# Optimization experiments

Measured on AMD Instinct MI355X. Metric: run time of the kernel, lower is better.

## Reference

```python
import jax, jax.numpy as jnp
import numpy as np

T, E, K, H, I = 512, 16, 4, 2880, 2880
G_H, G_I = H // 32, I // 32  # MXFP4 groups of 32 values (16 bytes/block)
ALPHA, LIMIT, EPS = 1.702, 7.0, 1e-5

FP4_VALUES = jnp.array([0.0, 0.5, 1.0, 1.5, 2.0, 3.0, 4.0, 6.0,
                        -0.0, -0.5, -1.0, -1.5, -2.0, -3.0, -4.0, -6.0], jnp.float32)


def dequant_mxfp4(blocks, scales):
    # blocks: uint8 [..., G, 16]; scales: uint8 [..., G] (biased exponent)
    pre = blocks.shape[:-2]
    G, B = blocks.shape[-2], blocks.shape[-1]
    lo = FP4_VALUES[(blocks & 0xF).astype(jnp.int32)]   # [..., G, B]
    hi = FP4_VALUES[(blocks >> 4).astype(jnp.int32)]    # [..., G, B]
    vals = jnp.stack([lo, hi], axis=-1).reshape(*pre, G, B * 2)  # interleave lo/hi per byte
    vals = jnp.ldexp(vals, (scales.astype(jnp.int32) - 127)[..., None])
    return vals.reshape(*pre, G * B * 2)


def swiglu(h):
    g = jnp.minimum(h[..., 0::2], LIMIT)
    l = jnp.clip(h[..., 1::2], -LIMIT, LIMIT)
    return g * jax.nn.sigmoid(ALPHA * g) * (l + 1.0)


def setup_inputs() -> dict:
    key = jax.random.key(0)
    ks = jax.random.split(key, 10)
    x = jax.random.normal(ks[0], (T, H), jnp.float32)
    norm_scale = jnp.ones((H,), jnp.float32)
    gate_w = jax.random.normal(ks[1], (E, H), jnp.float32) * 0.02
    gate_b = jnp.zeros((E,), jnp.float32)
    mlp1_blocks = jax.random.randint(ks[2], (E, 2 * I, G_H, 16), 0, 256, dtype=jnp.uint8)
    mlp1_scales = jax.random.randint(ks[3], (E, 2 * I, G_H), 118, 128, dtype=jnp.uint8)
    mlp1_bias = jax.random.normal(ks[4], (E, 2 * I), jnp.float32) * 0.02
    mlp2_blocks = jax.random.randint(ks[5], (E, H, G_I, 16), 0, 256, dtype=jnp.uint8)
    mlp2_scales = jax.random.randint(ks[6], (E, H, G_I), 118, 128, dtype=jnp.uint8)
    mlp2_bias = jax.random.normal(ks[7], (E, H), jnp.float32) * 0.02
    return {"x": x, "norm_scale": norm_scale, "gate_w": gate_w, "gate_b": gate_b,
            "mlp1_blocks": mlp1_blocks, "mlp1_scales": mlp1_scales, "mlp1_bias": mlp1_bias,
            "mlp2_blocks": mlp2_blocks, "mlp2_scales": mlp2_scales, "mlp2_bias": mlp2_bias}


def reference(x, norm_scale, gate_w, gate_b, mlp1_blocks, mlp1_scales, mlp1_bias,
              mlp2_blocks, mlp2_scales, mlp2_bias):
    # RMSNorm
    t = x * jax.lax.rsqrt(jnp.mean(x * x, axis=-1, keepdims=True) + EPS) * norm_scale
    # router: top-k + softmax over selected logits
    g = t @ gate_w.T + gate_b                      # [T, E]
    vals, idx = jax.lax.top_k(g, K)                # sorted, distinct indices
    w = jax.nn.softmax(vals, axis=-1)              # [T, K]
    n_tok = t.shape[0]
    route = jnp.zeros((n_tok, gate_w.shape[0]), t.dtype)
    route = route.at[jnp.arange(n_tok)[:, None], idx].set(w)  # [T, E] sparse weights
    # expert MLPs (dense dispatch; unrouted experts get zero weight)
    W1 = dequant_mxfp4(mlp1_blocks, mlp1_scales)   # [E, 2I, H]
    h = jnp.einsum('th,ech->tec', t, W1) + mlp1_bias[None]   # [T, E, 2I]
    h = swiglu(h)                                            # [T, E, I]
    W2 = dequant_mxfp4(mlp2_blocks, mlp2_scales)   # [E, H, I]
    o = jnp.einsum('tec,ehc->teh', h, W2) + mlp2_bias[None]  # [T, E, H]
    return x + jnp.einsum('teh,te->th', o, route)
```

## Files before the change

kernel.cpp:

```cpp
#include <hip/hip_runtime.h>
#include <hip/hip_bf16.h>

typedef __attribute__((ext_vector_type(8))) short short8;
typedef __attribute__((ext_vector_type(4))) float f32x4;
typedef __attribute__((ext_vector_type(4))) int i32x4;
typedef __attribute__((ext_vector_type(2))) int i32x2;
typedef __attribute__((ext_vector_type(4))) unsigned u32x4;

#define NTOK 512
#define NEXP 16
#define TOPK 4
#define HD   2880
#define ID   2880
#define N1   5760
#define NGRP 90
#define NKT  45
#define ROWB 5760

__device__ __forceinline__ unsigned perm(unsigned hi, unsigned lo, unsigned sel) {
  return __builtin_amdgcn_perm(hi, lo, sel);
}

__device__ __forceinline__ u32x4 dq_word4(unsigned p, unsigned hbl, unsigned hbh,
                                          unsigned lbl, unsigned lbh) {
  unsigned ph = p >> 4;
  unsigned il = p  & 0x07070707u, sl = p  & 0x08080808u;
  unsigned ih = ph & 0x07070707u, sh = ph & 0x08080808u;
  unsigned hbL = perm(hbh, hbl, il) | (sl << 4);
  unsigned lbL = perm(lbh, lbl, il);
  unsigned hbH = perm(hbh, hbl, ih) | (sh << 4);
  unsigned lbH = perm(lbh, lbl, ih);
  unsigned mL01 = perm(hbL, lbL, 0x05010400u);
  unsigned mL23 = perm(hbL, lbL, 0x07030602u);
  unsigned mH01 = perm(hbH, lbH, 0x05010400u);
  unsigned mH23 = perm(hbH, lbH, 0x07030602u);
  u32x4 w;
  w.x = perm(mH01, mL01, 0x05040100u);
  w.y = perm(mH01, mL01, 0x07060302u);
  w.z = perm(mH23, mL23, 0x05040100u);
  w.w = perm(mH23, mL23, 0x07060302u);
  return w;
}

__device__ __forceinline__ short8 dq_frag(unsigned pk, int sc) {
  unsigned m7 = (unsigned)((127 - sc) << 7);
  unsigned mm = m7 | (m7 << 16);
  unsigned e10 = (0x3F00u - m7) << 16;
  unsigned e32 = 0x3FC03F80u - mm;
  unsigned e54 = 0x40404000u - mm;
  unsigned e76 = 0x40C04080u - mm;
  unsigned hbl = perm(e32, e10, 0x07050301u);
  unsigned hbh = perm(e76, e54, 0x07050301u);
  unsigned lbl = perm(e32, e10, 0x06040200u);
  unsigned lbh = perm(e76, e54, 0x06040200u);
  u32x4 w = dq_word4(pk, hbl, hbh, lbl, lbh);
  return __builtin_bit_cast(short8, w);
}

__global__ __launch_bounds__(256)
void rmsnorm_k(const float* __restrict__ x, const float* __restrict__ nsc,
               float* __restrict__ tf, __hip_bfloat16* __restrict__ tb,
               int* __restrict__ cnt)
{
  int t = blockIdx.x;
  if (t == 0 && threadIdx.x < NEXP) cnt[threadIdx.x] = 0;
  const float* xr = x + (size_t)t * HD;
  float s = 0.f;
  for (int i = threadIdx.x; i < HD; i += 256) { float v = xr[i]; s += v * v; }
#pragma unroll
  for (int o = 32; o > 0; o >>= 1) s += __shfl_down(s, o);
  __shared__ float red[4];
  if ((threadIdx.x & 63) == 0) red[threadIdx.x >> 6] = s;
  __syncthreads();
  float tot = red[0] + red[1] + red[2] + red[3];
  float rinv = rsqrtf(tot / (float)HD + 1e-5f);
  for (int i = threadIdx.x; i < HD; i += 256) {
    float v = xr[i] * rinv * nsc[i];
    tf[(size_t)t * HD + i] = v;
    tb[(size_t)t * HD + i] = __float2bfloat16(v);
  }
}

__global__ __launch_bounds__(256)
void router_k(const float* __restrict__ tf, const float* __restrict__ gw,
              const float* __restrict__ gb, float* __restrict__ wpair,
              int* __restrict__ cnt, int* __restrict__ tok_list, int* __restrict__ pair_list)
{
  int t = blockIdx.x;
  int tid = threadIdx.x;
  int e = tid >> 4, l16 = tid & 15;
  const float* tr = tf + (size_t)t * HD;
  float s = 0.f;
  for (int i = l16; i < HD; i += 16) s += tr[i] * gw[e * HD + i];
#pragma unroll
  for (int o = 1; o < 16; o <<= 1) s += __shfl_xor(s, o);
  __shared__ float logits[NEXP];
  if (l16 == 0) logits[e] = s + gb[e];
  __syncthreads();
  if (tid == 0) {
    float v[NEXP];
#pragma unroll
    for (int i = 0; i < NEXP; ++i) v[i] = logits[i];
    int idx[TOPK]; float val[TOPK];
#pragma unroll
    for (int k = 0; k < TOPK; ++k) {
      int bi = 0; float bv = -1e30f;
      for (int i = 0; i < NEXP; ++i) if (v[i] > bv) { bv = v[i]; bi = i; }
      idx[k] = bi; val[k] = bv; v[bi] = -1e30f;
    }
    float mx = val[0], sum = 0.f, w[TOPK];
#pragma unroll
    for (int k = 0; k < TOPK; ++k) { w[k] = __expf(val[k] - mx); sum += w[k]; }
#pragma unroll
    for (int k = 0; k < TOPK; ++k) {
      float wk = w[k] / sum;
      int ee = idx[k];
      int slot = atomicAdd(&cnt[ee], 1);
      tok_list[ee * NTOK + slot]  = t;
      pair_list[ee * NTOK + slot] = t * TOPK + k;
      wpair[t * TOPK + k] = wk;
    }
  }
}

#define SYNC_LGKM do { asm volatile("s_waitcnt lgkmcnt(0)" ::: "memory"); \
    __builtin_amdgcn_sched_barrier(0); __builtin_amdgcn_s_barrier(); \
    __builtin_amdgcn_sched_barrier(0); } while (0)

template<int STAGE>
__global__ __launch_bounds__(256, 4)
void moe_gemm(const __hip_bfloat16* __restrict__ Asrc,
              const int* __restrict__ Bblk, const int* __restrict__ Bscl,
              const float* __restrict__ Bbias,
              const int* __restrict__ cnt,
              const int* __restrict__ tok_list, const int* __restrict__ pair_list,
              __hip_bfloat16* __restrict__ h_out, float* __restrict__ o_out)
{
  constexpr int NDIM = (STAGE == 1) ? N1 : HD;
  const int e  = blockIdx.z;
  const int ne = cnt[e];
  const int m0 = blockIdx.y * 128;
  if (m0 >= ne) return;
  const int n0 = blockIdx.x * 64;
  const int tid = threadIdx.x;
  const int wave = tid >> 6, lane = tid & 63;
  const int l15 = lane & 15, l4 = lane >> 4;

  __shared__ __align__(16) char Abuf[2][16384];

  const int* glist = (STAGE == 1 ? tok_list : pair_list) + e * NTOK;
  const int* plist = pair_list + e * NTOK;

  const char* agp[4];
  int awoff[4];
#pragma unroll
  for (int c = 0; c < 4; ++c) {
    int g    = c * 256 + tid;
    int row  = g >> 3;
    int cb   = (g & 7) * 16;
    int slot = m0 + row; if (slot > ne - 1) slot = ne - 1;
    agp[c]   = (const char*)Asrc + (size_t)glist[slot] * ROWB + cb;
    awoff[c] = row * 128 + (cb ^ ((row & 7) << 4));
  }

  const int wn = wave * 16;
  const int brow = n0 + wn + l15;
  const unsigned rb = (unsigned)(e * NDIM + brow) * NGRP;
  const unsigned bofs = rb * 16 + (unsigned)(l4 * 4);
  const unsigned srow = rb;

  int aoff[8][2];
#pragma unroll
  for (int mf = 0; mf < 8; ++mf) {
    int row = mf * 16 + l15;
#pragma unroll
    for (int kk = 0; kk < 2; ++kk)
      aoff[mf][kk] = row * 128 + ((kk * 64 + l4 * 16) ^ ((row & 7) << 4));
  }

  f32x4 zero = {0.f, 0.f, 0.f, 0.f};
  f32x4 acc[8];
#pragma unroll
  for (int a = 0; a < 8; ++a) acc[a] = zero;

  i32x4 Ar[4];
  unsigned q0, q1;
  int scx, scy;
  short8 b0, b1;

  auto loadB = [&](int tt) {
    i32x4 v0 = *(const i32x4*)(Bblk + bofs + (unsigned)((tt * 2 + 0) * 16));
    i32x4 v1 = *(const i32x4*)(Bblk + bofs + (unsigned)((tt * 2 + 1) * 16));
    q0 = (unsigned)(v0.x & 255) | ((unsigned)(v0.y & 255) << 8) |
         ((unsigned)(v0.z & 255) << 16) | ((unsigned)v0.w << 24);
    q1 = (unsigned)(v1.x & 255) | ((unsigned)(v1.y & 255) << 8) |
         ((unsigned)(v1.z & 255) << 16) | ((unsigned)v1.w << 24);
    i32x2 sv = *(const i32x2*)(Bscl + srow + (unsigned)(tt * 2));
    scx = sv.x; scy = sv.y;
  };

#pragma unroll
  for (int c = 0; c < 4; ++c) Ar[c] = *(const i32x4*)agp[c];
  loadB(0);
#pragma unroll
  for (int c = 0; c < 4; ++c) *(i32x4*)(Abuf[0] + awoff[c]) = Ar[c];
  b0 = dq_frag(q0, scx);
  b1 = dq_frag(q1, scy);
#pragma unroll
  for (int c = 0; c < 4; ++c) Ar[c] = *(const i32x4*)(agp[c] + 128);
  loadB(1);
  SYNC_LGKM;

  for (int t = 0; t < NKT; ++t) {
    const int cur = t & 1, nxt = cur ^ 1;
    int tld = t + 2; if (tld >= NKT) tld = NKT - 1;

#pragma unroll
    for (int c = 0; c < 4; ++c) *(i32x4*)(Abuf[nxt] + awoff[c]) = Ar[c];
#pragma unroll
    for (int c = 0; c < 4; ++c) Ar[c] = *(const i32x4*)(agp[c] + tld * 128);

    __builtin_amdgcn_s_setprio(1);
#pragma unroll
    for (int kk = 0; kk < 2; ++kk) {
      short8 bk = kk ? b1 : b0;
#pragma unroll
      for (int mf = 0; mf < 8; ++mf) {
        short8 af = *(const short8*)(Abuf[cur] + aoff[mf][kk]);
        acc[mf] = __builtin_amdgcn_mfma_f32_16x16x32_bf16(af, bk, acc[mf], 0, 0, 0);
      }
    }
    __builtin_amdgcn_s_setprio(0);

    b0 = dq_frag(q0, scx);
    b1 = dq_frag(q1, scy);
    loadB(tld);

    SYNC_LGKM;
  }

  if (STAGE == 1) {
#pragma unroll
    for (int ma = 0; ma < 8; ++ma) {
      int ncol = n0 + wn + l15;
      float bias = Bbias[e * NDIM + ncol];
#pragma unroll
      for (int j = 0; j < 4; ++j) {
        float u  = acc[ma][j] + bias;
        float up = __shfl_xor(u, 1);
        int slot = m0 + ma * 16 + l4 * 4 + j;
        if (!(lane & 1) && slot < ne) {
          float g  = fminf(u, 7.f);
          float lv = fminf(fmaxf(up, -7.f), 7.f);
          float hv = g / (1.f + __expf(-1.702f * g)) * (lv + 1.f);
          h_out[(size_t)plist[slot] * ID + (ncol >> 1)] = __float2bfloat16(hv);
        }
      }
    }
  } else {
#pragma unroll
    for (int ma = 0; ma < 8; ++ma) {
      int ncol = n0 + wn + l15;
      float bias = Bbias[e * NDIM + ncol];
#pragma unroll
      for (int j = 0; j < 4; ++j) {
        int slot = m0 + ma * 16 + l4 * 4 + j;
        if (slot < ne)
          o_out[(size_t)plist[slot] * HD + ncol] = acc[ma][j] + bias;
      }
    }
  }
}

__global__ __launch_bounds__(256)
void final_k(const float* __restrict__ x, const float* __restrict__ obuf,
             const float* __restrict__ wpair, float* __restrict__ out)
{
  int t = blockIdx.x;
  float w0 = wpair[t * 4 + 0], w1 = wpair[t * 4 + 1];
  float w2 = wpair[t * 4 + 2], w3 = wpair[t * 4 + 3];
  const float* o0 = obuf + (size_t)(t * 4) * HD;
  for (int i = threadIdx.x; i < HD; i += 256) {
    float r = x[(size_t)t * HD + i]
            + w0 * o0[i] + w1 * o0[HD + i] + w2 * o0[2 * HD + i] + w3 * o0[3 * HD + i];
    out[(size_t)t * HD + i] = r;
  }
}

extern "C" void kernel_launch(void* const* d_in, const int* in_sizes, int n_in,
                              void* d_out, int out_size, void* d_ws, size_t ws_size,
                              hipStream_t stream)
{
  const float* x    = (const float*)d_in[0];
  const float* nsc  = (const float*)d_in[1];
  const float* gw   = (const float*)d_in[2];
  const float* gb   = (const float*)d_in[3];
  const int*   b1   = (const int*)d_in[4];
  const int*   s1   = (const int*)d_in[5];
  const float* bia1 = (const float*)d_in[6];
  const int*   b2   = (const int*)d_in[7];
  const int*   s2   = (const int*)d_in[8];
  const float* bia2 = (const float*)d_in[9];
  float* out = (float*)d_out;

  char* ws = (char*)d_ws;
  size_t off = 0;
  auto alloc = [&](size_t bytes) {
    char* p = ws + off;
    off = (off + bytes + 255) & ~(size_t)255;
    return p;
  };
  float*           tf    = (float*)alloc((size_t)NTOK * HD * 4);
  __hip_bfloat16*  tb    = (__hip_bfloat16*)alloc((size_t)NTOK * HD * 2);
  __hip_bfloat16*  hbuf  = (__hip_bfloat16*)alloc((size_t)NTOK * TOPK * ID * 2);
  float*           obuf  = (float*)alloc((size_t)NTOK * TOPK * HD * 4);
  float*           wpair = (float*)alloc(NTOK * TOPK * 4);
  int*             cnt   = (int*)alloc(64);
  int*             tokl  = (int*)alloc(NEXP * NTOK * 4);
  int*             pairl = (int*)alloc(NEXP * NTOK * 4);

  rmsnorm_k<<<NTOK, 256, 0, stream>>>(x, nsc, tf, tb, cnt);
  router_k<<<NTOK, 256, 0, stream>>>(tf, gw, gb, wpair, cnt, tokl, pairl);
  moe_gemm<1><<<dim3(N1 / 64, 4, NEXP), 256, 0, stream>>>(tb, b1, s1, bia1, cnt, tokl, pairl, hbuf, nullptr);
  moe_gemm<2><<<dim3(HD / 64, 4, NEXP), 256, 0, stream>>>(hbuf, b2, s2, bia2, cnt, tokl, pairl, nullptr, obuf);
  final_k<<<NTOK, 256, 0, stream>>>(x, obuf, wpair, out);
}
```

Before: 479.8 us.

## Deepen B-weight prefetch to three stages with rotating register sets

```diff
diff --git a/kernel.cpp b/kernel.cpp
--- a/kernel.cpp
+++ b/kernel.cpp
@@ -57,6 +57,11 @@
   return __builtin_bit_cast(short8, w);
 }
 
+__device__ __forceinline__ unsigned pack8(i32x4 v) {
+  return (unsigned)(v.x & 255) | ((unsigned)(v.y & 255) << 8) |
+         ((unsigned)(v.z & 255) << 16) | ((unsigned)v.w << 24);
+}
+
 __global__ __launch_bounds__(256)
 void rmsnorm_k(const float* __restrict__ x, const float* __restrict__ nsc,
                float* __restrict__ tf, __hip_bfloat16* __restrict__ tb,
@@ -128,7 +133,7 @@
     __builtin_amdgcn_sched_barrier(0); } while (0)
 
 template<int STAGE>
-__global__ __launch_bounds__(256, 4)
+__global__ __launch_bounds__(256, 3)
 void moe_gemm(const __hip_bfloat16* __restrict__ Asrc,
               const int* __restrict__ Bblk, const int* __restrict__ Bscl,
               const float* __restrict__ Bbias,
@@ -184,60 +189,62 @@
   for (int a = 0; a < 8; ++a) acc[a] = zero;
 
   i32x4 Ar[4];
-  unsigned q0, q1;
-  int scx, scy;
+  i32x4 q0a, q0b; i32x2 s0;
+  i32x4 q1a, q1b; i32x2 s1;
+  i32x4 q2a, q2b; i32x2 s2;
   short8 b0, b1;
 
-  auto loadB = [&](int tt) {
-    i32x4 v0 = *(const i32x4*)(Bblk + bofs + (unsigned)((tt * 2 + 0) * 16));
-    i32x4 v1 = *(const i32x4*)(Bblk + bofs + (unsigned)((tt * 2 + 1) * 16));
-    q0 = (unsigned)(v0.x & 255) | ((unsigned)(v0.y & 255) << 8) |
-         ((unsigned)(v0.z & 255) << 16) | ((unsigned)v0.w << 24);
-    q1 = (unsigned)(v1.x & 255) | ((unsigned)(v1.y & 255) << 8) |
-         ((unsigned)(v1.z & 255) << 16) | ((unsigned)v1.w << 24);
-    i32x2 sv = *(const i32x2*)(Bscl + srow + (unsigned)(tt * 2));
-    scx = sv.x; scy = sv.y;
-  };
+#define LOADB(QA, QB, SS, tt) do { \
+    QA = *(const i32x4*)(Bblk + bofs + (unsigned)(((tt) * 2 + 0) * 16)); \
+    QB = *(const i32x4*)(Bblk + bofs + (unsigned)(((tt) * 2 + 1) * 16)); \
+    SS = *(const i32x2*)(Bscl + srow + (unsigned)((tt) * 2)); } while (0)
 
 #pragma unroll
   for (int c = 0; c < 4; ++c) Ar[c] = *(const i32x4*)agp[c];
-  loadB(0);
+  LOADB(q0a, q0b, s0, 0);
+  LOADB(q1a, q1b, s1, 1);
+  LOADB(q2a, q2b, s2, 2);
 #pragma unroll
   for (int c = 0; c < 4; ++c) *(i32x4*)(Abuf[0] + awoff[c]) = Ar[c];
-  b0 = dq_frag(q0, scx);
-  b1 = dq_frag(q1, scy);
+  b0 = dq_frag(pack8(q0a), s0.x);
+  b1 = dq_frag(pack8(q0b), s0.y);
 #pragma unroll
   for (int c = 0; c < 4; ++c) Ar[c] = *(const i32x4*)(agp[c] + 128);
-  loadB(1);
   SYNC_LGKM;
 
-  for (int t = 0; t < NKT; ++t) {
-    const int cur = t & 1, nxt = cur ^ 1;
-    int tld = t + 2; if (tld >= NKT) tld = NKT - 1;
-
-#pragma unroll
-    for (int c = 0; c < 4; ++c) *(i32x4*)(Abuf[nxt] + awoff[c]) = Ar[c];
-#pragma unroll
-    for (int c = 0; c < 4; ++c) Ar[c] = *(const i32x4*)(agp[c] + tld * 128);
-
-    __builtin_amdgcn_s_setprio(1);
-#pragma unroll
-    for (int kk = 0; kk < 2; ++kk) {
-      short8 bk = kk ? b1 : b0;
-#pragma unroll
-      for (int mf = 0; mf < 8; ++mf) {
-        short8 af = *(const short8*)(Abuf[cur] + aoff[mf][kk]);
-        acc[mf] = __builtin_amdgcn_mfma_f32_16x16x32_bf16(af, bk, acc[mf], 0, 0, 0);
-      }
-    }
-    __builtin_amdgcn_s_setprio(0);
-
-    b0 = dq_frag(q0, scx);
-    b1 = dq_frag(q1, scy);
-    loadB(tld);
-
-    SYNC_LGKM;
-  }
+#define BODY(t, QDa, QDb, SD, QFa, QFb, SF) do { \
+    const int cur = (t) & 1, nxt = cur ^ 1; \
+    int tldA = (t) + 2; if (tldA >= NKT) tldA = NKT - 1; \
+    int tldB = (t) + 3; if (tldB >= NKT) tldB = NKT - 1; \
+    _Pragma("unroll") \
+    for (int c = 0; c < 4; ++c) *(i32x4*)(Abuf[nxt] + awoff[c]) = Ar[c]; \
+    _Pragma("unroll") \
+    for (int c = 0; c < 4; ++c) Ar[c] = *(const i32x4*)(agp[c] + tldA * 128); \
+    __builtin_amdgcn_s_setprio(1); \
+    _Pragma("unroll") \
+    for (int kk = 0; kk < 2; ++kk) { \
+      short8 bk = kk ? b1 : b0; \
+      _Pragma("unroll") \
+      for (int mf = 0; mf < 8; ++mf) { \
+        short8 af = *(const short8*)(Abuf[cur] + aoff[mf][kk]); \
+        acc[mf] = __builtin_amdgcn_mfma_f32_16x16x32_bf16(af, bk, acc[mf], 0, 0, 0); \
+      } \
+    } \
+    __builtin_amdgcn_s_setprio(0); \
+    b0 = dq_frag(pack8(QDa), SD.x); \
+    b1 = dq_frag(pack8(QDb), SD.y); \
+    LOADB(QFa, QFb, SF, tldB); \
+    SYNC_LGKM; \
+  } while (0)
+
+  for (int tp = 0; tp < NKT / 3; ++tp) {
+    const int t = 3 * tp;
+    BODY(t + 0, q1a, q1b, s1, q0a, q0b, s0);
+    BODY(t + 1, q2a, q2b, s2, q1a, q1b, s1);
+    BODY(t + 2, q0a, q0b, s0, q2a, q2b, s2);
+  }
+#undef BODY
+#undef LOADB
 
   if (STAGE == 1) {
 #pragma unroll
```

After: 467.7 us. 2.5% less time.

## Stage A, B and scales through a 3-slot LDS ring via async global_load_lds

Applied to the files above, without the earlier changes.

```diff
diff --git a/kernel.cpp b/kernel.cpp
--- a/kernel.cpp
+++ b/kernel.cpp
@@ -16,6 +16,20 @@
 #define NGRP 90
 #define NKT  45
 #define ROWB 5760
+
+#define SLOT  25600
+#define A_OFF 0
+#define B_OFF 16384
+#define S_OFF 24576
+
+__device__ __forceinline__ void async16(void* lds, const void* g) {
+  __builtin_amdgcn_global_load_lds((const __attribute__((address_space(1))) unsigned*)g,
+                                   (__attribute__((address_space(3))) unsigned*)lds, 16, 0, 0);
+}
+__device__ __forceinline__ void async4(void* lds, const void* g) {
+  __builtin_amdgcn_global_load_lds((const __attribute__((address_space(1))) unsigned*)g,
+                                   (__attribute__((address_space(3))) unsigned*)lds, 4, 0, 0);
+}
 
 __device__ __forceinline__ unsigned perm(unsigned hi, unsigned lo, unsigned sel) {
   return __builtin_amdgcn_perm(hi, lo, sel);
@@ -57,6 +71,11 @@
   return __builtin_bit_cast(short8, w);
 }
 
+__device__ __forceinline__ unsigned pack8(i32x4 v) {
+  return (unsigned)(v.x & 255) | ((unsigned)(v.y & 255) << 8) |
+         ((unsigned)(v.z & 255) << 16) | ((unsigned)v.w << 24);
+}
+
 __global__ __launch_bounds__(256)
 void rmsnorm_k(const float* __restrict__ x, const float* __restrict__ nsc,
                float* __restrict__ tf, __hip_bfloat16* __restrict__ tb,
@@ -123,12 +142,10 @@
   }
 }
 
-#define SYNC_LGKM do { asm volatile("s_waitcnt lgkmcnt(0)" ::: "memory"); \
-    __builtin_amdgcn_sched_barrier(0); __builtin_amdgcn_s_barrier(); \
-    __builtin_amdgcn_sched_barrier(0); } while (0)
+#define FENCE __builtin_amdgcn_sched_barrier(0)
 
 template<int STAGE>
-__global__ __launch_bounds__(256, 4)
+__global__ __launch_bounds__(256)
 void moe_gemm(const __hip_bfloat16* __restrict__ Asrc,
               const int* __restrict__ Bblk, const int* __restrict__ Bscl,
               const float* __restrict__ Bbias,
@@ -137,6 +154,7 @@
               __hip_bfloat16* __restrict__ h_out, float* __restrict__ o_out)
 {
   constexpr int NDIM = (STAGE == 1) ? N1 : HD;
+  __shared__ __align__(16) char ring[3 * SLOT];
   const int e  = blockIdx.z;
   const int ne = cnt[e];
   const int m0 = blockIdx.y * 128;
@@ -146,28 +164,34 @@
   const int wave = tid >> 6, lane = tid & 63;
   const int l15 = lane & 15, l4 = lane >> 4;
 
-  __shared__ __align__(16) char Abuf[2][16384];
-
   const int* glist = (STAGE == 1 ? tok_list : pair_list) + e * NTOK;
   const int* plist = pair_list + e * NTOK;
 
   const char* agp[4];
-  int awoff[4];
+  int alds[4];
 #pragma unroll
   for (int c = 0; c < 4; ++c) {
-    int g    = c * 256 + tid;
-    int row  = g >> 3;
-    int cb   = (g & 7) * 16;
+    int o   = c * 4096 + tid * 16;
+    int row = o >> 7;
+    int scb = (o & 127) ^ ((row & 7) << 4);
     int slot = m0 + row; if (slot > ne - 1) slot = ne - 1;
-    agp[c]   = (const char*)Asrc + (size_t)glist[slot] * ROWB + cb;
-    awoff[c] = row * 128 + (cb ^ ((row & 7) << 4));
-  }
-
-  const int wn = wave * 16;
-  const int brow = n0 + wn + l15;
-  const unsigned rb = (unsigned)(e * NDIM + brow) * NGRP;
-  const unsigned bofs = rb * 16 + (unsigned)(l4 * 4);
-  const unsigned srow = rb;
+    agp[c]  = (const char*)Asrc + (size_t)glist[slot] * ROWB + scb;
+    alds[c] = A_OFF + c * 4096 + wave * 1024;
+  }
+  const char* bgp[2];
+  int blds[2];
+#pragma unroll
+  for (int c = 0; c < 2; ++c) {
+    int idx = c * 256 + tid;
+    int row = idx >> 3, ch = idx & 7;
+    bgp[c]  = (const char*)Bblk + (size_t)(e * NDIM + n0 + row) * ROWB
+              + ((ch ^ (row & 7)) * 16);
+    blds[c] = B_OFF + c * 4096 + wave * 1024;
+  }
+  int sidx = tid < 128 ? tid : 127;
+  const char* sgp = (const char*)Bscl +
+      ((size_t)(e * NDIM + n0 + (sidx >> 1)) * NGRP + (sidx & 1)) * 4;
+  const int slds = S_OFF + wave * 256;
 
   int aoff[8][2];
 #pragma unroll
@@ -175,50 +199,49 @@
     int row = mf * 16 + l15;
 #pragma unroll
     for (int kk = 0; kk < 2; ++kk)
-      aoff[mf][kk] = row * 128 + ((kk * 64 + l4 * 16) ^ ((row & 7) << 4));
-  }
+      aoff[mf][kk] = A_OFF + row * 128 + ((kk * 64 + l4 * 16) ^ ((row & 7) << 4));
+  }
+  const int brow = wave * 16 + l15;
+  int boff[2];
+#pragma unroll
+  for (int kk = 0; kk < 2; ++kk)
+    boff[kk] = B_OFF + brow * 128 + ((kk * 64 + l4 * 16) ^ ((brow & 7) << 4));
+  const int soff = S_OFF + brow * 8;
 
   f32x4 zero = {0.f, 0.f, 0.f, 0.f};
   f32x4 acc[8];
 #pragma unroll
   for (int a = 0; a < 8; ++a) acc[a] = zero;
 
-  i32x4 Ar[4];
-  unsigned q0, q1;
-  int scx, scy;
-  short8 b0, b1;
-
-  auto loadB = [&](int tt) {
-    i32x4 v0 = *(const i32x4*)(Bblk + bofs + (unsigned)((tt * 2 + 0) * 16));
-    i32x4 v1 = *(const i32x4*)(Bblk + bofs + (unsigned)((tt * 2 + 1) * 16));
-    q0 = (unsigned)(v0.x & 255) | ((unsigned)(v0.y & 255) << 8) |
-         ((unsigned)(v0.z & 255) << 16) | ((unsigned)v0.w << 24);
-    q1 = (unsigned)(v1.x & 255) | ((unsigned)(v1.y & 255) << 8) |
-         ((unsigned)(v1.z & 255) << 16) | ((unsigned)v1.w << 24);
-    i32x2 sv = *(const i32x2*)(Bscl + srow + (unsigned)(tt * 2));
-    scx = sv.x; scy = sv.y;
-  };
-
-#pragma unroll
-  for (int c = 0; c < 4; ++c) Ar[c] = *(const i32x4*)agp[c];
-  loadB(0);
-#pragma unroll
-  for (int c = 0; c < 4; ++c) *(i32x4*)(Abuf[0] + awoff[c]) = Ar[c];
-  b0 = dq_frag(q0, scx);
-  b1 = dq_frag(q1, scy);
-#pragma unroll
-  for (int c = 0; c < 4; ++c) Ar[c] = *(const i32x4*)(agp[c] + 128);
-  loadB(1);
-  SYNC_LGKM;
-
+#define ISSUE(tt, sl) do { char* sb_ = ring + (sl) * SLOT; \
+    _Pragma("unroll") \
+    for (int c_ = 0; c_ < 4; ++c_) async16(sb_ + alds[c_], agp[c_] + (tt) * 128); \
+    _Pragma("unroll") \
+    for (int c_ = 0; c_ < 2; ++c_) async16(sb_ + blds[c_], bgp[c_] + (tt) * 128); \
+    async4(sb_ + slds, sgp + (tt) * 8); } while (0)
+
+  ISSUE(0, 0);
+  ISSUE(1, 1);
+  FENCE;
+
+  int sl_issue = 2, sl_cons = 0;
   for (int t = 0; t < NKT; ++t) {
-    const int cur = t & 1, nxt = cur ^ 1;
     int tld = t + 2; if (tld >= NKT) tld = NKT - 1;
-
-#pragma unroll
-    for (int c = 0; c < 4; ++c) *(i32x4*)(Abuf[nxt] + awoff[c]) = Ar[c];
-#pragma unroll
-    for (int c = 0; c < 4; ++c) Ar[c] = *(const i32x4*)(agp[c] + tld * 128);
+    ISSUE(tld, sl_issue);
+    sl_issue = (sl_issue == 2) ? 0 : sl_issue + 1;
+    FENCE;
+    asm volatile("s_waitcnt vmcnt(14)" ::: "memory");
+    FENCE;
+    __builtin_amdgcn_s_barrier();
+    FENCE;
+
+    const char* sb = ring + sl_cons * SLOT;
+    sl_cons = (sl_cons == 2) ? 0 : sl_cons + 1;
+    i32x2 sc = *(const i32x2*)(sb + soff);
+    i32x4 braw0 = *(const i32x4*)(sb + boff[0]);
+    i32x4 braw1 = *(const i32x4*)(sb + boff[1]);
+    short8 b0 = dq_frag(pack8(braw0), sc.x);
+    short8 b1 = dq_frag(pack8(braw1), sc.y);
 
     __builtin_amdgcn_s_setprio(1);
 #pragma unroll
@@ -226,19 +249,18 @@
       short8 bk = kk ? b1 : b0;
 #pragma unroll
       for (int mf = 0; mf < 8; ++mf) {
-        short8 af = *(const short8*)(Abuf[cur] + aoff[mf][kk]);
+        short8 af = *(const short8*)(sb + aoff[mf][kk]);
         acc[mf] = __builtin_amdgcn_mfma_f32_16x16x32_bf16(af, bk, acc[mf], 0, 0, 0);
       }
     }
     __builtin_amdgcn_s_setprio(0);
-
-    b0 = dq_frag(q0, scx);
-    b1 = dq_frag(q1, scy);
-    loadB(tld);
-
-    SYNC_LGKM;
-  }
-
+    FENCE;
+    __builtin_amdgcn_s_barrier();
+    FENCE;
+  }
+#undef ISSUE
+
+  const int wn = wave * 16;
   if (STAGE == 1) {
 #pragma unroll
     for (int ma = 0; ma < 8; ++ma) {
```

Measured after the change: 448.0 us. -6.6%, faster.
